# Kernel tuning notes

Measured on AMD Instinct MI355X. Metric: run time of the kernel, lower is better.

The kernel has to match this reference:

```python
import jax, jax.numpy as jnp
import numpy as np

B, N, D, M, K, H = 8, 196, 512, 20, 77, 8
SPARSITY_RATIO = 0.1


def _ln(x, g, b, eps=1e-5):
    mu = x.mean(axis=-1, keepdims=True)
    var = ((x - mu) ** 2).mean(axis=-1, keepdims=True)
    return (x - mu) / jnp.sqrt(var + eps) * g + b


def setup_inputs() -> dict:
    key = jax.random.key(0)
    ks = jax.random.split(key, 8)
    s = lambda i, shape, sc=1.0: jax.random.normal(ks[i], shape, jnp.float32) * sc
    return {
        "F_clean": s(0, (B, N, D)),
        "text_features": s(1, (K, D)),
        "in_proj_w": s(2, (3 * D, D), 0.02),
        "in_proj_b": jnp.zeros((3 * D,), jnp.float32),
        "out_w": s(3, (D, D), 0.02),
        "out_b": jnp.zeros((D,), jnp.float32),
        "ln1_g": jnp.ones((D,), jnp.float32),
        "ln1_b": jnp.zeros((D,), jnp.float32),
        "ln2_g": jnp.ones((D,), jnp.float32),
        "ln2_b": jnp.zeros((D,), jnp.float32),
        "mlp_w1": s(4, (D, D), 0.02),
        "mlp_b1": jnp.zeros((D,), jnp.float32),
        "mlp_ln_g": jnp.ones((D,), jnp.float32),
        "mlp_ln_b": jnp.zeros((D,), jnp.float32),
        "mlp_w2": s(5, (M, D), 0.02),
        "mlp_b2": jnp.zeros((M,), jnp.float32),
        "templates": s(6, (M, D)),
    }


def reference(F_clean, text_features, in_proj_w, in_proj_b, out_w, out_b,
              ln1_g, ln1_b, ln2_g, ln2_b,
              mlp_w1, mlp_b1, mlp_ln_g, mlp_ln_b, mlp_w2, mlp_b2, templates):
    hd = D // H
    text_exp = jnp.broadcast_to(text_features[None], (B, K, D))
    q_in = _ln(text_exp, ln1_g, ln1_b)
    k_in = _ln(F_clean, ln1_g, ln1_b)
    Wq, Wk, Wv = in_proj_w[:D], in_proj_w[D:2 * D], in_proj_w[2 * D:]
    bq, bk, bv = in_proj_b[:D], in_proj_b[D:2 * D], in_proj_b[2 * D:]
    q = (q_in @ Wq.T + bq).reshape(B, K, H, hd).transpose(0, 2, 1, 3)
    k = (k_in @ Wk.T + bk).reshape(B, N, H, hd).transpose(0, 2, 1, 3)
    v = (F_clean @ Wv.T + bv).reshape(B, N, H, hd).transpose(0, 2, 1, 3)
    scores = jnp.einsum('bhkd,bhnd->bhkn', q, k) / jnp.sqrt(jnp.float32(hd))
    attn = jax.nn.softmax(scores, axis=-1)                     # [B,H,K,N]
    ctx = jnp.einsum('bhkn,bhnd->bhkd', attn, v)
    ctx = ctx.transpose(0, 2, 1, 3).reshape(B, K, D)
    attn_output = ctx @ out_w.T + out_b
    attn_weights = attn.mean(axis=1)                           # [B,K,N]
    attn_output = _ln(attn_output, ln2_g, ln2_b)

    # Vectorized form of the per-patch loop (j over N)
    w = attn_weights.transpose(0, 2, 1)[..., None]             # [B,N,K,1]
    interact = F_clean[:, :, None, :] * attn_output[:, None, :, :]  # [B,N,K,D]
    weighted = interact * w
    clean = weighted - weighted.mean(axis=2, keepdims=True)
    h = clean @ mlp_w1.T + mlp_b1
    h = _ln(h, mlp_ln_g, mlp_ln_b)
    h = jax.nn.gelu(h, approximate=False)
    comps = h @ mlp_w2.T + mlp_b2                              # [B,N,K,M]
    Q_patch = (comps * w).sum(axis=2)                          # [B,N,M]

    # Outer-product construct: [B,N,D,M]
    Q = F_clean[..., None] * templates.T[None, None] * Q_patch[:, :, None, :]

    # Top-k sparsify along D, then L2-normalize along D
    k_keep = max(int(D * SPARSITY_RATIO), 1)
    Qr = Q.transpose(0, 1, 3, 2).reshape(B * N * M, D)
    _, idx = jax.lax.top_k(jnp.abs(Qr), k_keep)
    rows = jnp.arange(B * N * M)[:, None]
    mask = jnp.zeros_like(Qr).at[rows, idx].set(1.0)
    Qs = (Qr * mask).reshape(B, N, M, D).transpose(0, 1, 3, 2)
    nrm = jnp.maximum(jnp.linalg.norm(Qs, axis=2, keepdims=True), 1e-6)
    return (Qs / nrm, attn_weights)
```

## Files before the change

### kernel.cpp

```cpp
#include <hip/hip_runtime.h>
#include <hip/hip_bf16.h>
#include <math.h>


typedef unsigned int uint;
typedef _Float16 f16x8 __attribute__((ext_vector_type(8)));
typedef float f32x4 __attribute__((ext_vector_type(4)));

#define DI __device__ __forceinline__

DI float wsumf(float v){ for(int o=32;o>0;o>>=1) v += __shfl_xor(v,o,64); return v; }
DI int   wsumi(int v){ for(int o=32;o>0;o>>=1) v += __shfl_xor(v,o,64); return v; }
DI float wmaxf(float v){ for(int o=32;o>0;o>>=1) v = fmaxf(v,__shfl_xor(v,o,64)); return v; }

__global__ __launch_bounds__(256) void k0_transpose(const float* ipw, const float* ow, const float* mw1,
                             float* WT, float* OWT, _Float16* w1hi, _Float16* w1lo){
  int bid = blockIdx.x;
  if(bid < 768){
    __shared__ float t[32][33];
    int tdin = bid & 15, tdout = bid >> 4;
    int tx = threadIdx.x & 31, ty = threadIdx.x >> 5;
    int dout0 = tdout*32, din0 = tdin*32;
    for(int r=ty; r<32; r+=8) t[r][tx] = ipw[(size_t)(dout0+r)*512 + din0+tx];
    __syncthreads();
    for(int r=ty; r<32; r+=8) WT[(size_t)(din0+r)*1536 + dout0+tx] = t[tx][r];
  } else if(bid < 1024){
    __shared__ float t[32][33];
    int b2 = bid - 768;
    int tdin = b2 & 15, tdout = b2 >> 4;
    int tx = threadIdx.x & 31, ty = threadIdx.x >> 5;
    int dout0 = tdout*32, din0 = tdin*32;
    for(int r=ty; r<32; r+=8) t[r][tx] = ow[(size_t)(dout0+r)*512 + din0+tx];
    __syncthreads();
    for(int r=ty; r<32; r+=8) OWT[(size_t)(din0+r)*512 + dout0+tx] = t[tx][r];
  } else {
    int i3 = (bid-1024)*256 + threadIdx.x;
    int t = i3&7, ln = (i3>>3)&63, J = (i3>>9)&31, T = i3>>14;
    int j = J*16 + (ln&15);
    int d = T*32 + ((ln>>4)<<3) + t;
    float w = mw1[j*512 + d] * 64.0f;
    _Float16 hi = (_Float16)w;
    _Float16 lo = (_Float16)(w - (float)hi);
    w1hi[i3] = hi; w1lo[i3] = lo;
  }
}

__global__ __launch_bounds__(256) void k1_q(const float* text, const float* ipb,
                                            const float* g1, const float* b1p,
                                            const float* WT, float* qws){
  int k = blockIdx.x >> 1, half = blockIdx.x & 1;
  int tid = threadIdx.x;
  __shared__ float xln[512];
  __shared__ float rA[4], rB[4];
  float x0 = text[k*512+tid], x1 = text[k*512+256+tid];
  float s1 = wsumf(x0+x1), s2 = wsumf(x0*x0+x1*x1);
  int w = tid>>6, ln = tid&63;
  if(!ln){ rA[w]=s1; rB[w]=s2; }
  __syncthreads();
  float mu = (rA[0]+rA[1]+rA[2]+rA[3])*(1.f/512.f);
  float var = (rB[0]+rB[1]+rB[2]+rB[3])*(1.f/512.f) - mu*mu;
  float rs = 1.f/sqrtf(fmaxf(var,0.f) + 1e-5f);
  xln[tid]     = (x0-mu)*rs*g1[tid]     + b1p[tid];
  xln[tid+256] = (x1-mu)*rs*g1[tid+256] + b1p[tid+256];
  __syncthreads();
  int d = half*256 + tid;
  float a0=0.f,a1=0.f,a2=0.f,a3=0.f;
  for(int din=0; din<512; din+=4){
    a0 += xln[din  ] * WT[(din  )*1536 + d];
    a1 += xln[din+1] * WT[(din+1)*1536 + d];
    a2 += xln[din+2] * WT[(din+2)*1536 + d];
    a3 += xln[din+3] * WT[(din+3)*1536 + d];
  }
  qws[k*512+d] = ipb[d] + ((a0+a1)+(a2+a3));
}

__global__ __launch_bounds__(512) void k2_kv(const float* F, const float* ipb,
                                             const float* g1, const float* b1p,
                                             const float* WT, float* kmat, float* vmat){
  int r0 = blockIdx.x*8; int tid = threadIdx.x;
  __shared__ float xs[8][512];
  __shared__ float xl[8][512];
  __shared__ float red[8][64];
  __shared__ float mu8[8], rs8[8];
  for(int e=tid; e<4096; e+=512){ int r=e>>9, d=e&511; xs[r][d] = F[(size_t)(r0+r)*512 + d]; }
  __syncthreads();
  {
    int r = tid>>6, t = tid&63; float s=0.f, q=0.f;
    for(int i=0;i<8;++i){ float v = xs[r][t+64*i]; s+=v; q+=v*v; }
    red[r][t] = s; __syncthreads();
    if(tid<8){ float ss=0; for(int i=0;i<64;++i) ss+=red[tid][i]; mu8[tid]=ss*(1.f/512.f); }
    __syncthreads();
    red[r][t] = q; __syncthreads();
    if(tid<8){ float qq=0; for(int i=0;i<64;++i) qq+=red[tid][i];
      float m=mu8[tid]; rs8[tid]=1.f/sqrtf(fmaxf(qq*(1.f/512.f)-m*m,0.f)+1e-5f); }
    __syncthreads();
  }
  for(int e=tid; e<4096; e+=512){ int r=e>>9, d=e&511;
    xl[r][d] = (xs[r][d]-mu8[r])*rs8[r]*g1[d] + b1p[d]; }
  __syncthreads();
  int d=tid;
  float ak[8], av[8];
  float bk=ipb[512+d], bv=ipb[1024+d];
  #pragma unroll
  for(int r=0;r<8;++r){ ak[r]=bk; av[r]=bv; }
  for(int din=0; din<512; din+=4){
    float wk[4], wv[4];
    #pragma unroll
    for(int u=0;u<4;++u){ wk[u]=WT[(din+u)*1536+512+d]; wv[u]=WT[(din+u)*1536+1024+d]; }
    #pragma unroll
    for(int r=0;r<8;++r){
      float4 a4 = *(const float4*)&xl[r][din];
      float4 x4 = *(const float4*)&xs[r][din];
      ak[r] += a4.x*wk[0]+a4.y*wk[1]+a4.z*wk[2]+a4.w*wk[3];
      av[r] += x4.x*wv[0]+x4.y*wv[1]+x4.z*wv[2]+x4.w*wv[3];
    }
  }
  #pragma unroll
  for(int r=0;r<8;++r){
    size_t base = (size_t)(r0+r)*512;
    kmat[base+d]=ak[r]; vmat[base+d]=av[r];
  }
}

__global__ __launch_bounds__(256) void k3_attn(const float* qws, const float* kmat, float* attf){
  int bid = blockIdx.x;
  int kc = bid>>6, b = (bid>>3)&7, h = bid&7;
  int tid = threadIdx.x; int n = tid; int w = tid>>6, ln = tid&63;
  __shared__ float qb[8][64];
  __shared__ float rM[8][4], rS[8][4];
  float4 kr[16];
  if(n < 196){
    const float4* kp = (const float4*)(kmat + ((size_t)(b*196+n))*512 + h*64);
    #pragma unroll
    for(int j=0;j<16;++j) kr[j] = kp[j];
  }
  int kbase = kc*8;
  for(int e=tid; e<512; e+=256){ int kk=e>>6, j=e&63; int k=kbase+kk;
    qb[kk][j] = (k<77)? qws[k*512 + h*64 + j] : 0.f; }
  __syncthreads();
  float sc[8];
  #pragma unroll
  for(int kk=0;kk<8;++kk){
    float s = 0.f;
    if(n<196){
      const float4* q4 = (const float4*)qb[kk];
      #pragma unroll
      for(int j=0;j<16;++j){ float4 q = q4[j];
        s += q.x*kr[j].x + q.y*kr[j].y + q.z*kr[j].z + q.w*kr[j].w; }
      sc[kk] = s*0.125f;
    } else sc[kk] = -INFINITY;
  }
  #pragma unroll
  for(int kk=0;kk<8;++kk){ float m = wmaxf(sc[kk]); if(!ln) rM[kk][w]=m; }
  __syncthreads();
  float ex[8];
  #pragma unroll
  for(int kk=0;kk<8;++kk){
    float m = fmaxf(fmaxf(rM[kk][0],rM[kk][1]),fmaxf(rM[kk][2],rM[kk][3]));
    float e = expf(sc[kk]-m);
    ex[kk]=e;
    float s = wsumf(e); if(!ln) rS[kk][w]=s;
  }
  __syncthreads();
  #pragma unroll
  for(int kk=0;kk<8;++kk){
    int k = kbase+kk;
    if(k<77 && n<196){
      float tot = rS[kk][0]+rS[kk][1]+rS[kk][2]+rS[kk][3];
      attf[(((size_t)(b*8+h))*77 + k)*196 + n] = ex[kk]/tot;
    }
  }
}

__global__ __launch_bounds__(256) void k4_ctx(const float* attf, const float* vmat, float* ctx){
  int bid = blockIdx.x;
  int kc = bid>>6, b = (bid>>3)&7, h = bid&7;
  int tid = threadIdx.x; int ng = tid>>6, j = tid&63;
  __shared__ float vT[196][64];
  __shared__ float aT[8][196];
  __shared__ float red[8][4][64];
  for(int e=tid; e<196*16; e+=256){ int n=e>>4, jc=e&15;
    const float4* vp = (const float4*)(vmat + ((size_t)(b*196+n))*512 + h*64);
    *(float4*)&vT[n][jc*4] = vp[jc];
  }
  int kbase=kc*8;
  for(int e=tid; e<8*196; e+=256){ int kk=e/196, n=e-kk*196; int k=kbase+kk;
    aT[kk][n] = (k<77)? attf[(((size_t)(b*8+h))*77+k)*196+n] : 0.f; }
  __syncthreads();
  float vr[49];
  #pragma unroll
  for(int t=0;t<49;++t) vr[t] = vT[ng*49+t][j];
  #pragma unroll
  for(int kk=0;kk<8;++kk){
    float p=0.f;
    #pragma unroll
    for(int t=0;t<49;++t) p += aT[kk][ng*49+t]*vr[t];
    red[kk][ng][j]=p;
  }
  __syncthreads();
  for(int e=tid; e<512; e+=256){ int kk=e>>6, j2=e&63; int k=kbase+kk;
    if(k<77){
      float s = red[kk][0][j2]+red[kk][1][j2]+red[kk][2][j2]+red[kk][3][j2];
      ctx[((size_t)(b*77+k))*512 + h*64 + j2] = s;
    } }
}

__global__ void k5_attw(const float* attf, float* attw, float* out2){
  int idx = blockIdx.x*256+threadIdx.x;
  if(idx >= 8*77*196) return;
  int b = idx / (77*196); int rem = idx - b*(77*196);
  float s=0.f;
  #pragma unroll
  for(int h=0;h<8;++h) s += attf[((size_t)(b*8+h))*77*196 + rem];
  s *= 0.125f;
  attw[idx]=s; out2[idx]=s;
}

__global__ __launch_bounds__(512) void k6_ao(const float* ctx, const float* OWT,
                                             const float* ob, const float* g2, const float* b2p,
                                             float* AO){
  int R0 = blockIdx.x*8; int tid = threadIdx.x;
  __shared__ float xs[8][512];
  __shared__ float ao[8][512];
  __shared__ float red[8][64];
  __shared__ float mu8[8], rs8[8];
  for(int e=tid;e<4096;e+=512){ int r=e>>9,d=e&511; xs[r][d]=ctx[(size_t)(R0+r)*512+d]; }
  __syncthreads();
  int d=tid;
  float a[8]; float obv=ob[d];
  #pragma unroll
  for(int r=0;r<8;++r) a[r]=obv;
  for(int din=0;din<512;din+=4){
    float wv[4];
    #pragma unroll
    for(int u=0;u<4;++u) wv[u]=OWT[(din+u)*512+d];
    #pragma unroll
    for(int r=0;r<8;++r){
      float4 x4 = *(const float4*)&xs[r][din];
      a[r] += x4.x*wv[0]+x4.y*wv[1]+x4.z*wv[2]+x4.w*wv[3];
    }
  }
  #pragma unroll
  for(int r=0;r<8;++r) ao[r][d]=a[r];
  __syncthreads();
  {
    int r=tid>>6,t=tid&63; float s=0.f,q=0.f;
    for(int i=0;i<8;++i){ float v=ao[r][t+64*i]; s+=v; q+=v*v; }
    red[r][t]=s; __syncthreads();
    if(tid<8){ float ss=0; for(int i=0;i<64;++i) ss+=red[tid][i]; mu8[tid]=ss*(1.f/512.f); }
    __syncthreads(); red[r][t]=q; __syncthreads();
    if(tid<8){ float qq=0; for(int i=0;i<64;++i) qq+=red[tid][i];
      float m=mu8[tid]; rs8[tid]=1.f/sqrtf(fmaxf(qq*(1.f/512.f)-m*m,0.f)+1e-5f); }
    __syncthreads();
  }
  for(int e=tid;e<4096;e+=512){ int r=e>>9,dd=e&511;
    AO[(size_t)(R0+r)*512+dd] = (ao[r][dd]-mu8[r])*rs8[r]*g2[dd] + b2p[dd]; }
}

__global__ __launch_bounds__(512) void k6b_sv(const float* AO, const float* attw,
                                              float* Svws, float* wsumws){
  int bid = blockIdx.x;
  int b = bid/25, nt = bid - b*25;
  int n0 = nt*8;
  int tid = threadIdx.x;
  __shared__ float wsK[80][8];
  for(int e=tid; e<640; e+=512){ int k=e>>3, r=e&7; int n=n0+r;
    wsK[k][r] = (k<77 && n<196)? attw[((size_t)(b*77+k))*196 + n] : 0.f; }
  __syncthreads();
  if(tid<8){ int n=n0+tid;
    if(n<196){ float s=0.f;
      for(int k=0;k<77;++k) s+=wsK[k][tid];
      wsumws[b*196+n]=s; } }
  int d = tid;
  float acc[8];
  #pragma unroll
  for(int r=0;r<8;++r) acc[r]=0.f;
  const float* aob = AO + (size_t)b*77*512 + d;
  for(int k=0;k<77;++k){
    float a = aob[(size_t)k*512];
    #pragma unroll
    for(int r=0;r<8;++r) acc[r] += wsK[k][r]*a;
  }
  #pragma unroll
  for(int r=0;r<8;++r){ int n=n0+r; if(n<196)
    Svws[((size_t)(b*196+n))*512 + d] = acc[r]*(1.f/77.f); }
}

struct __align__(16) K7Smem {
  _Float16 Ah[2*16*512];
  _Float16 Al[2*16*512];
  float b1s[512], gs[512], bs[512];
  float wvS[80];
  float redS[8][32], redQ[8][32];
  float muA[32], rsA[32];
  float gfin[512];
  float qred[320];
};

#define K7_MFMA3(ACC, AFH, AFL, BH, BL) \
  ACC = __builtin_amdgcn_mfma_f32_16x16x32_f16(AFL, BH, ACC, 0,0,0); \
  ACC = __builtin_amdgcn_mfma_f32_16x16x32_f16(AFH, BL, ACC, 0,0,0); \
  ACC = __builtin_amdgcn_mfma_f32_16x16x32_f16(AFH, BH, ACC, 0,0,0);

struct Bset { f16x8 h0,h1,h2,h3,l0,l1,l2,l3; };

DI void loadB(Bset& s, const _Float16* bph, const _Float16* bpl, int t){
  const _Float16* ph = bph + t*16384;
  const _Float16* pl = bpl + t*16384;
  s.h0 = *(const f16x8*)(ph);       s.h1 = *(const f16x8*)(ph+512);
  s.h2 = *(const f16x8*)(ph+1024);  s.h3 = *(const f16x8*)(ph+1536);
  s.l0 = *(const f16x8*)(pl);       s.l1 = *(const f16x8*)(pl+512);
  s.l2 = *(const f16x8*)(pl+1024);  s.l3 = *(const f16x8*)(pl+1536);
}

template<int MT>
DI void stepMFMA(f32x4 acc[][4], const _Float16* Ah, const _Float16* Al,
                 const Bset& B, int t, int ln){
  #pragma unroll
  for(int mt=0; mt<MT; ++mt){
    int off = (mt*16 + t)*512 + ((ln + t)&63)*8;
    f16x8 fh = *(const f16x8*)&Ah[off];
    f16x8 fl = *(const f16x8*)&Al[off];
    K7_MFMA3(acc[mt][0], fh, fl, B.h0, B.l0)
    K7_MFMA3(acc[mt][1], fh, fl, B.h1, B.l1)
    K7_MFMA3(acc[mt][2], fh, fl, B.h2, B.l2)
    K7_MFMA3(acc[mt][3], fh, fl, B.h3, B.l3)
  }
}

template<int MT, int K0>
DI void k7_body(int bn, const float* F, const float* AO, const float* attw,
                const _Float16* w1hi, const _Float16* w1lo,
                const float* b1p, const float* lng, const float* lnb,
                const float* w2, const float* b2p,
                const float* Svws, const float* wsumws,
                float* Qpws, K7Smem& sm){
  int b = bn/196, n = bn - b*196;
  int tid = threadIdx.x; int w = tid>>6, ln = tid&63;
  int col = ln&15, quad = ln>>4;
  const float* AObase = AO + (size_t)b*77*512;
  sm.b1s[tid] = b1p[tid]; sm.gs[tid] = lng[tid]; sm.bs[tid] = lnb[tid];
  if(tid<80) sm.wvS[tid] = (tid<77)? attw[((size_t)(b*77+tid))*196+n] : 0.f;
  __syncthreads();

  {
    int d0 = (tid&63)*8;
    int r0 = tid>>6;
    int t  = d0>>5;
    int k8 = (d0&31)>>3;
    float4 f0 = *(const float4*)&F[(size_t)bn*512 + d0];
    float4 f1 = *(const float4*)&F[(size_t)bn*512 + d0+4];
    float4 sv0 = *(const float4*)&Svws[(size_t)bn*512 + d0];
    float4 sv1 = *(const float4*)&Svws[(size_t)bn*512 + d0+4];
    float fk[8] = {f0.x*1024.f,f0.y*1024.f,f0.z*1024.f,f0.w*1024.f,
                   f1.x*1024.f,f1.y*1024.f,f1.z*1024.f,f1.w*1024.f};
    float sv[8] = {sv0.x,sv0.y,sv0.z,sv0.w,sv1.x,sv1.y,sv1.z,sv1.w};
    #pragma unroll
    for(int it=0; it<MT*2; ++it){
      int row = r0 + it*8;
      int grow = K0 + row;
      bool ok = grow < 77;
      int rl = ok ? grow : 0;
      float wm = ok ? sm.wvS[grow] : 0.f;
      const float* ap = AObase + (size_t)rl*512 + d0;
      float4 a0 = *(const float4*)ap;
      float4 a1 = *(const float4*)(ap+4);
      float av[8] = {a0.x,a0.y,a0.z,a0.w,a1.x,a1.y,a1.z,a1.w};
      f16x8 hfrag, lfrag;
      #pragma unroll
      for(int i=0;i<8;++i){
        float c = ok ? fk[i]*(wm*av[i] - sv[i]) : 0.f;
        _Float16 h = (_Float16)c;
        hfrag[i] = h;
        lfrag[i] = (_Float16)(c - (float)h);
      }
      int lane = (row&15) | (k8<<4);
      int pos = (lane + t)&63;
      int idx = (((row>>4)*16 + t)*512) + pos*8;
      *(f16x8*)&sm.Ah[idx] = hfrag;
      *(f16x8*)&sm.Al[idx] = lfrag;
    }
  }
  __syncthreads();
  f32x4 acc[MT][4];
  #pragma unroll
  for(int mt=0;mt<MT;++mt)
    #pragma unroll
    for(int jj=0;jj<4;++jj) acc[mt][jj] = (f32x4){0.f,0.f,0.f,0.f};

  const _Float16* bph = w1hi + ((w*4)*64 + ln)*8;
  const _Float16* bpl = w1lo + ((w*4)*64 + ln)*8;

  Bset s0, s1;
  loadB(s0, bph, bpl, 0);
  #pragma unroll 1
  for(int tt=0; tt<16; tt+=2){
    loadB(s1, bph, bpl, tt+1);
    stepMFMA<MT>(acc, sm.Ah, sm.Al, s0, tt, ln);
    if(tt+2<16) loadB(s0, bph, bpl, tt+2);
    stepMFMA<MT>(acc, sm.Ah, sm.Al, s1, tt+1, ln);
  }

  const float UNS = 1.f/65536.f;
  #pragma unroll
  for(int mt=0;mt<MT;++mt){
    float s[4]={0.f,0.f,0.f,0.f}, q[4]={0.f,0.f,0.f,0.f};
    #pragma unroll
    for(int jj=0;jj<4;++jj){
      int j = w*64 + jj*16 + col; float bj = sm.b1s[j];
      #pragma unroll
      for(int r=0;r<4;++r){
        float h = acc[mt][jj][r]*UNS + bj;
        s[r]+=h; q[r]+=h*h;
      }
    }
    #pragma unroll
    for(int r=0;r<4;++r){
      #pragma unroll
      for(int o=1;o<16;o<<=1){ s[r]+=__shfl_xor(s[r],o,64); q[r]+=__shfl_xor(q[r],o,64); }
    }
    if(col==0){
      #pragma unroll
      for(int r=0;r<4;++r){ int row = mt*16+quad*4+r; sm.redS[w][row]=s[r]; sm.redQ[w][row]=q[r]; }
    }
  }
  __syncthreads();
  if(tid<MT*16){
    float s=0.f,q=0.f;
    #pragma unroll
    for(int ww=0;ww<8;++ww){ s+=sm.redS[ww][tid]; q+=sm.redQ[ww][tid]; }
    float mu = s*(1.f/512.f);
    float var = q*(1.f/512.f)-mu*mu;
    sm.muA[tid]=mu; sm.rsA[tid]=1.f/sqrtf(fmaxf(var,0.f)+1e-5f);
  }
  __syncthreads();
  float gp[4]={0.f,0.f,0.f,0.f};
  #pragma unroll
  for(int mt=0;mt<MT;++mt){
    #pragma unroll
    for(int r=0;r<4;++r){
      int lr = mt*16+quad*4+r;
      float mu=sm.muA[lr], rs=sm.rsA[lr], wk=sm.wvS[K0+lr];
      #pragma unroll
      for(int jj=0;jj<4;++jj){
        int j = w*64 + jj*16 + col;
        float h = acc[mt][jj][r]*UNS + sm.b1s[j];
        float x = (h-mu)*rs;
        float y = x*sm.gs[j]+sm.bs[j];
        float gl = 0.5f*y*(1.f+erff(y*0.70710678118654752f));
        gp[jj] += wk*gl;
      }
    }
  }
  #pragma unroll
  for(int jj=0;jj<4;++jj){ gp[jj]+=__shfl_xor(gp[jj],16,64); gp[jj]+=__shfl_xor(gp[jj],32,64); }
  if(ln<16){
    #pragma unroll
    for(int jj=0;jj<4;++jj) sm.gfin[w*64 + jj*16 + ln] = gp[jj];
  }
  __syncthreads();
  if(tid<320){ int m=tid>>4, seg=tid&15; float p=0.f;
    for(int u=0;u<32;++u){ int j=seg*32+u; p += sm.gfin[j]*w2[m*512+j]; }
    sm.qred[m*16+seg]=p; }
  __syncthreads();
  if(tid<20){ float s=0.f;
    for(int seg=0;seg<16;++seg) s+=sm.qred[tid*16+seg];
    if(K0==0) s += b2p[tid]*wsumws[bn];
    Qpws[(size_t)bn*60 + (K0==0?0:(K0==32?20:40)) + tid]=s; }
}

__global__
__attribute__((amdgpu_flat_work_group_size(512,512)))
void k7_mlp(const float* F, const float* AO, const float* attw,
            const _Float16* w1hi, const _Float16* w1lo,
            const float* b1p, const float* lng, const float* lnb,
            const float* w2, const float* b2p,
            const float* Svws, const float* wsumws,
            float* Qpws){
  __shared__ K7Smem sm;
  int bid = blockIdx.x;
  int bn = bid/3;
  int third = bid - bn*3;
  if(third==0)      k7_body<2,0 >(bn,F,AO,attw,w1hi,w1lo,b1p,lng,lnb,w2,b2p,Svws,wsumws,Qpws,sm);
  else if(third==1) k7_body<2,32>(bn,F,AO,attw,w1hi,w1lo,b1p,lng,lnb,w2,b2p,Svws,wsumws,Qpws,sm);
  else              k7_body<1,64>(bn,F,AO,attw,w1hi,w1lo,b1p,lng,lnb,w2,b2p,Svws,wsumws,Qpws,sm);
}

__global__ __launch_bounds__(256) void k8_topk(const float* F, const float* T,
                                               const float* Qpws, float* out1){
  int bn = blockIdx.x; int tid = threadIdx.x;
  int w = tid>>6, ln = tid&63;
  __shared__ float Fv[512];
  __shared__ float QpS[20];
  __shared__ float ninv[20];
  __shared__ unsigned char selb[20][64];
  for(int e=tid;e<512;e+=256) Fv[e]=F[(size_t)bn*512+e];
  if(tid<20) QpS[tid]=Qpws[(size_t)bn*60+tid] + Qpws[(size_t)bn*60+20+tid] + Qpws[(size_t)bn*60+40+tid];
  __syncthreads();
  for(int rr=0; rr<5; ++rr){
    int m = rr*4 + w;
    float qv[8]; uint key[8];
    const float4* tp = (const float4*)(T + (size_t)m*512 + ln*8);
    float4 t0 = tp[0], t1 = tp[1];
    float tf[8] = {t0.x,t0.y,t0.z,t0.w,t1.x,t1.y,t1.z,t1.w};
    float qp = QpS[m];
    #pragma unroll
    for(int i=0;i<8;++i){ float p = Fv[ln*8+i]*tf[i]; qv[i]=p*qp;
      key[i]=__float_as_uint(qv[i])&0x7fffffffu; }
    uint th=0u;
    for(int bit=30; bit>=0; --bit){
      uint cand = th | (1u<<bit);
      int c=0;
      #pragma unroll
      for(int i=0;i<8;++i) c += (key[i]>=cand);
      c = wsumi(c);
      if(c>=51) th=cand;
    }
    int cg=0;
    #pragma unroll
    for(int i=0;i<8;++i) cg += (key[i]>th);
    cg = wsumi(cg);
    int rneed = 51-cg;
    int eqc=0;
    #pragma unroll
    for(int i=0;i<8;++i) eqc += (key[i]==th);
    int pre=eqc;
    for(int o=1;o<64;o<<=1){ int v=__shfl_up(pre,o,64); if(ln>=o) pre+=v; }
    pre -= eqc;
    unsigned char mbits=0; float ss=0.f; int rk=pre;
    #pragma unroll
    for(int i=0;i<8;++i){
      bool s;
      if(key[i]>th) s=true;
      else if(key[i]==th){ s = (rk<rneed); rk++; }
      else s=false;
      if(s){ mbits |= (unsigned char)(1u<<i); ss += qv[i]*qv[i]; }
    }
    ss = wsumf(ss);
    if(ln==0) ninv[m] = 1.f/fmaxf(sqrtf(ss),1e-6f);
    selb[m][ln]=mbits;
  }
  __syncthreads();
  size_t base=(size_t)bn*10240;
  for(int e=tid;e<10240;e+=256){
    int d=e/20, mm=e-d*20;
    float val=0.f;
    if((selb[mm][d>>3]>>(d&7))&1){
      val = Fv[d]*T[(size_t)mm*512+d]*QpS[mm]*ninv[mm];
    }
    out1[base+e]=val;
  }
}

extern "C" void kernel_launch(void* const* d_in, const int* in_sizes, int n_in,
                              void* d_out, int out_size, void* d_ws, size_t ws_size,
                              hipStream_t stream){
  const float* F    = (const float*)d_in[0];
  const float* text = (const float*)d_in[1];
  const float* ipw  = (const float*)d_in[2];
  const float* ipb  = (const float*)d_in[3];
  const float* outw = (const float*)d_in[4];
  const float* outb = (const float*)d_in[5];
  const float* g1   = (const float*)d_in[6];
  const float* b1   = (const float*)d_in[7];
  const float* g2   = (const float*)d_in[8];
  const float* b2   = (const float*)d_in[9];
  const float* mw1  = (const float*)d_in[10];
  const float* mb1  = (const float*)d_in[11];
  const float* mlg  = (const float*)d_in[12];
  const float* mlb  = (const float*)d_in[13];
  const float* mw2  = (const float*)d_in[14];
  const float* mb2  = (const float*)d_in[15];
  const float* tmpl = (const float*)d_in[16];
  float* ws = (float*)d_ws;
  float* WT   = ws;
  float* OWT  = ws +  786432;
  float* qws  = ws + 1048576;
  float* kmat = ws + 1088000;
  float* vmat = ws + 1890816;
  float* attf = ws + 2693632;
  float* attw = ws + 3659520;
  float* ctx  = ws + 3780256;
  float* AO   = ws + 4095648;
  _Float16* w1hi = (_Float16*)(ws + 4473760);
  _Float16* w1lo = (_Float16*)(ws + 4604832);
  float* wsum = ws + 1048576;
  float* Sv   = ws + 1088000;
  float* Qp   = ws +  786432;
  float* out1 = (float*)d_out;
  float* out2 = out1 + 16056320;

  hipLaunchKernelGGL(k0_transpose, dim3(2048), dim3(256), 0, stream, ipw, outw, mw1, WT, OWT, w1hi, w1lo);
  hipLaunchKernelGGL(k1_q,   dim3(154), dim3(256), 0, stream, text, ipb, g1, b1, WT, qws);
  hipLaunchKernelGGL(k2_kv,  dim3(196), dim3(512), 0, stream, F, ipb, g1, b1, WT, kmat, vmat);
  hipLaunchKernelGGL(k3_attn,dim3(640), dim3(256), 0, stream, qws, kmat, attf);
  hipLaunchKernelGGL(k4_ctx, dim3(640), dim3(256), 0, stream, attf, vmat, ctx);
  hipLaunchKernelGGL(k5_attw,dim3(472), dim3(256), 0, stream, attf, attw, out2);
  hipLaunchKernelGGL(k6_ao,  dim3(77),  dim3(512), 0, stream, ctx, OWT, outb, g2, b2, AO);
  hipLaunchKernelGGL(k6b_sv, dim3(200), dim3(512), 0, stream, AO, attw, Sv, wsum);
  hipLaunchKernelGGL(k7_mlp, dim3(4704),dim3(512), 0, stream, F, AO, attw, w1hi, w1lo, mb1, mlg, mlb, mw2, mb2, Sv, wsum, Qp);
  hipLaunchKernelGGL(k8_topk,dim3(1568),dim3(256), 0, stream, F, tmpl, Qp, out1);
}
```

Measured before the change: 688.1 us.

## Halve k2_kv rows per block, deepen k7 B prefetch, use ballot counts in topk

k2_kv now handles 4 rows per block instead of 8, so it launches 392 blocks instead of 196 and fills more compute units, at the cost of reading the weight matrix twice as often. The k7 MFMA loop moves from double to quadruple buffering of B fragments to hide more global load latency, which raises register pressure. The w2 reduction staggers its start index by segment, apparently to spread accesses across banks. The top-k threshold search replaces a shuffle-based wave sum with a ballot plus popcount, which cuts cross-lane reduction steps in the bitwise radix loop.

```diff
diff --git a/kernel.cpp b/kernel.cpp
--- a/kernel.cpp
+++ b/kernel.cpp
@@ -77,38 +77,43 @@
 __global__ __launch_bounds__(512) void k2_kv(const float* F, const float* ipb,
                                              const float* g1, const float* b1p,
                                              const float* WT, float* kmat, float* vmat){
-  int r0 = blockIdx.x*8; int tid = threadIdx.x;
-  __shared__ float xs[8][512];
-  __shared__ float xl[8][512];
-  __shared__ float red[8][64];
-  __shared__ float mu8[8], rs8[8];
-  for(int e=tid; e<4096; e+=512){ int r=e>>9, d=e&511; xs[r][d] = F[(size_t)(r0+r)*512 + d]; }
+  int r0 = blockIdx.x*4; int tid = threadIdx.x;
+  __shared__ float xs[4][512];
+  __shared__ float xl[4][512];
+  __shared__ float red[4][64];
+  __shared__ float mu4[4], rs4[4];
+  for(int e=tid; e<2048; e+=512){ int r=e>>9, d=e&511; xs[r][d] = F[(size_t)(r0+r)*512 + d]; }
   __syncthreads();
   {
-    int r = tid>>6, t = tid&63; float s=0.f, q=0.f;
-    for(int i=0;i<8;++i){ float v = xs[r][t+64*i]; s+=v; q+=v*v; }
-    red[r][t] = s; __syncthreads();
-    if(tid<8){ float ss=0; for(int i=0;i<64;++i) ss+=red[tid][i]; mu8[tid]=ss*(1.f/512.f); }
+    float s=0.f, q=0.f; int r=0, t=0;
+    if(tid<256){
+      r = tid>>6; t = tid&63;
+      for(int i=0;i<8;++i){ float v = xs[r][t+64*i]; s+=v; q+=v*v; }
+      red[r][t] = s;
+    }
     __syncthreads();
-    red[r][t] = q; __syncthreads();
-    if(tid<8){ float qq=0; for(int i=0;i<64;++i) qq+=red[tid][i];
-      float m=mu8[tid]; rs8[tid]=1.f/sqrtf(fmaxf(qq*(1.f/512.f)-m*m,0.f)+1e-5f); }
+    if(tid<4){ float ss=0; for(int i=0;i<64;++i) ss+=red[tid][i]; mu4[tid]=ss*(1.f/512.f); }
     __syncthreads();
-  }
-  for(int e=tid; e<4096; e+=512){ int r=e>>9, d=e&511;
-    xl[r][d] = (xs[r][d]-mu8[r])*rs8[r]*g1[d] + b1p[d]; }
+    if(tid<256) red[r][t] = q;
+    __syncthreads();
+    if(tid<4){ float qq=0; for(int i=0;i<64;++i) qq+=red[tid][i];
+      float m=mu4[tid]; rs4[tid]=1.f/sqrtf(fmaxf(qq*(1.f/512.f)-m*m,0.f)+1e-5f); }
+    __syncthreads();
+  }
+  for(int e=tid; e<2048; e+=512){ int r=e>>9, d=e&511;
+    xl[r][d] = (xs[r][d]-mu4[r])*rs4[r]*g1[d] + b1p[d]; }
   __syncthreads();
   int d=tid;
-  float ak[8], av[8];
+  float ak[4], av[4];
   float bk=ipb[512+d], bv=ipb[1024+d];
   #pragma unroll
-  for(int r=0;r<8;++r){ ak[r]=bk; av[r]=bv; }
+  for(int r=0;r<4;++r){ ak[r]=bk; av[r]=bv; }
   for(int din=0; din<512; din+=4){
     float wk[4], wv[4];
     #pragma unroll
     for(int u=0;u<4;++u){ wk[u]=WT[(din+u)*1536+512+d]; wv[u]=WT[(din+u)*1536+1024+d]; }
     #pragma unroll
-    for(int r=0;r<8;++r){
+    for(int r=0;r<4;++r){
       float4 a4 = *(const float4*)&xl[r][din];
       float4 x4 = *(const float4*)&xs[r][din];
       ak[r] += a4.x*wk[0]+a4.y*wk[1]+a4.z*wk[2]+a4.w*wk[3];
@@ -116,7 +121,7 @@
     }
   }
   #pragma unroll
-  for(int r=0;r<8;++r){
+  for(int r=0;r<4;++r){
     size_t base = (size_t)(r0+r)*512;
     kmat[base+d]=ak[r]; vmat[base+d]=av[r];
   }
@@ -391,14 +396,19 @@
   const _Float16* bph = w1hi + ((w*4)*64 + ln)*8;
   const _Float16* bpl = w1lo + ((w*4)*64 + ln)*8;
 
-  Bset s0, s1;
+  Bset s0, s1, s2, s3;
   loadB(s0, bph, bpl, 0);
+  loadB(s1, bph, bpl, 1);
   #pragma unroll 1
-  for(int tt=0; tt<16; tt+=2){
-    loadB(s1, bph, bpl, tt+1);
+  for(int tt=0; tt<16; tt+=4){
+    loadB(s2, bph, bpl, tt+2);
     stepMFMA<MT>(acc, sm.Ah, sm.Al, s0, tt, ln);
-    if(tt+2<16) loadB(s0, bph, bpl, tt+2);
+    loadB(s3, bph, bpl, tt+3);
     stepMFMA<MT>(acc, sm.Ah, sm.Al, s1, tt+1, ln);
+    if(tt+4<16) loadB(s0, bph, bpl, tt+4);
+    stepMFMA<MT>(acc, sm.Ah, sm.Al, s2, tt+2, ln);
+    if(tt+5<16) loadB(s1, bph, bpl, tt+5);
+    stepMFMA<MT>(acc, sm.Ah, sm.Al, s3, tt+3, ln);
   }
 
   const float UNS = 1.f/65536.f;
@@ -460,7 +470,8 @@
   }
   __syncthreads();
   if(tid<320){ int m=tid>>4, seg=tid&15; float p=0.f;
-    for(int u=0;u<32;++u){ int j=seg*32+u; p += sm.gfin[j]*w2[m*512+j]; }
+    for(int u=0;u<32;++u){ int uu=(u+seg)&31; int j=seg*32+uu;
+      p += sm.gfin[j]*w2[m*512+j]; }
     sm.qred[m*16+seg]=p; }
   __syncthreads();
   if(tid<20){ float s=0.f;
@@ -512,14 +523,12 @@
       uint cand = th | (1u<<bit);
       int c=0;
       #pragma unroll
-      for(int i=0;i<8;++i) c += (key[i]>=cand);
-      c = wsumi(c);
+      for(int i=0;i<8;++i) c += (int)__popcll(__ballot(key[i]>=cand));
       if(c>=51) th=cand;
     }
     int cg=0;
     #pragma unroll
-    for(int i=0;i<8;++i) cg += (key[i]>th);
-    cg = wsumi(cg);
+    for(int i=0;i<8;++i) cg += (int)__popcll(__ballot(key[i]>th));
     int rneed = 51-cg;
     int eqc=0;
     #pragma unroll
@@ -592,7 +601,7 @@
 
   hipLaunchKernelGGL(k0_transpose, dim3(2048), dim3(256), 0, stream, ipw, outw, mw1, WT, OWT, w1hi, w1lo);
   hipLaunchKernelGGL(k1_q,   dim3(154), dim3(256), 0, stream, text, ipb, g1, b1, WT, qws);
-  hipLaunchKernelGGL(k2_kv,  dim3(196), dim3(512), 0, stream, F, ipb, g1, b1, WT, kmat, vmat);
+  hipLaunchKernelGGL(k2_kv,  dim3(392), dim3(512), 0, stream, F, ipb, g1, b1, WT, kmat, vmat);
   hipLaunchKernelGGL(k3_attn,dim3(640), dim3(256), 0, stream, qws, kmat, attf);
   hipLaunchKernelGGL(k4_ctx, dim3(640), dim3(256), 0, stream, attf, vmat, ctx);
   hipLaunchKernelGGL(k5_attw,dim3(472), dim3(256), 0, stream, attf, attw, out2);
```

New measurement: 669.1 us. 2.8% less time.
